# Performance work log

Measured on AMD Instinct MI355X. Metric: run time of the kernel, lower is better.

The kernel has to match this reference:

```python
import jax, jax.numpy as jnp
import numpy as np

B, T, IN_DIM, HID_DIM = 64, 1024, 256, 256


def setup_inputs() -> dict:
    key = jax.random.key(0)
    ks = jax.random.split(key, 5)
    glorot = np.sqrt(6.0 / (IN_DIM + HID_DIM * 2)).astype(np.float32)
    def W(k):
        return jax.random.uniform(k, (IN_DIM + HID_DIM, HID_DIM), jnp.float32, -glorot, glorot)
    return {
        "x": jax.random.normal(ks[0], (B, T, IN_DIM), jnp.float32),
        "W_i": W(ks[1]), "b_i": jnp.zeros((HID_DIM,), jnp.float32),
        "W_f": W(ks[2]), "b_f": jnp.zeros((HID_DIM,), jnp.float32),
        "W_o": W(ks[3]), "b_o": jnp.zeros((HID_DIM,), jnp.float32),
        "W_c": W(ks[4]), "b_c": jnp.zeros((HID_DIM,), jnp.float32),
    }


def reference(x, W_i, b_i, W_f, b_f, W_o, b_o, W_c, b_c):
    # x: [B, T, in_dim] -> time-major [T, B, in_dim]
    xt = jnp.transpose(x, (1, 0, 2))
    batch = x.shape[0]
    c0 = jnp.zeros((batch, HID_DIM), x.dtype)
    h0 = jnp.zeros((batch, HID_DIM), x.dtype)

    def step(carry, x_t):
        c, h = carry
        hx = jnp.concatenate([h, x_t], axis=1)  # [B, hid+in]
        i = jax.nn.sigmoid(hx @ W_i + b_i)
        f = jax.nn.sigmoid(hx @ W_f + b_f)
        o = jax.nn.sigmoid(hx @ W_o + b_o)
        c_new = f * c + i * jnp.tanh(hx @ W_c + b_c)
        h_new = o * jnp.tanh(c_new)
        return (c_new, h_new), h_new

    _, outputs = jax.lax.scan(step, (c0, h0), xt)
    return outputs  # [T, B, hid_dim]
```

## Files before the change

### kernel.cpp

```cpp
#include <hip/hip_runtime.h>
#include <hip/hip_fp16.h>
#include <cstdint>

typedef _Float16 f16x8 __attribute__((ext_vector_type(8)));
typedef _Float16 half2_t __attribute__((ext_vector_type(2)));
typedef float f32x4 __attribute__((ext_vector_type(4)));
typedef uint32_t u32x4 __attribute__((ext_vector_type(4)));
typedef uint32_t u32x2 __attribute__((ext_vector_type(2)));


#define XG_OFF    0ULL
#define XG_BYTES  134217728ULL
#define AP_OFF    (XG_OFF + XG_BYTES)
#define AP_BYTES  33554432ULL
#define BP_OFF    (AP_OFF + AP_BYTES)
#define BP_BYTES  524288ULL
#define WHPQ_OFF  (BP_OFF + BP_BYTES)
#define WHPQ_BYTES 425984ULL
#define WLG_OFF   (WHPQ_OFF + WHPQ_BYTES)
#define WLG_BYTES 98304ULL
#define BIAS_OFF  (WLG_OFF + WLG_BYTES)

__device__ inline half2_t u2h2(uint32_t v) {
    union { uint32_t u; half2_t h; } c; c.u = v; return c.h;
}
#define FD(W, H, A) __builtin_amdgcn_fdot2(u2h2(W), u2h2(H), (A), false)
#define QB(v, pat) __int_as_float(__builtin_amdgcn_ds_swizzle(__float_as_int(v), (pat)))

#define QLIST(F) F(0) F(1) F(2) F(3) F(4) F(5) F(6) F(7) F(8) F(9) F(10) F(11) F(12) \
                 F(13) F(14) F(15) F(16) F(17) F(18) F(19) F(20) F(21) F(22) F(23) F(24) F(25)

__global__ void pack_weights(const float* __restrict__ Wi, const float* __restrict__ Wf,
                             const float* __restrict__ Wo, const float* __restrict__ Wc,
                             const float* __restrict__ bi, const float* __restrict__ bf,
                             const float* __restrict__ bo, const float* __restrict__ bc,
                             uint32_t* __restrict__ WhpQ, uint32_t* __restrict__ WlG,
                             __half* __restrict__ Bp, float* __restrict__ bias_eff)
{
    int tidg = blockIdx.x * blockDim.x + threadIdx.x;
    if (tidg < 106496) {
        int i = tidg & 3;
        int c = (tidg >> 2) & 1023;
        int q = tidg >> 12;
        int kp = q * 4 + i;
        int u = c >> 2, g = c & 3;
        const float* W = (g == 0) ? Wi : (g == 1) ? Wf : (g == 2) ? Wo : Wc;
        union { uint32_t u32; __half h[2]; } pk;
        pk.h[0] = __float2half(W[(2 * kp) * 256 + u]);
        pk.h[1] = __float2half(W[(2 * kp + 1) * 256 + u]);
        WhpQ[tidg] = pk.u32;
    } else if (tidg < 131072) {
        int e = tidg - 106496;
        int k = e & 1;
        int c = (e >> 1) & 1023;
        int jp = e >> 11;
        int kp = 104 + 2 * jp + k;
        int u = c >> 2, g = c & 3;
        const float* W = (g == 0) ? Wi : (g == 1) ? Wf : (g == 2) ? Wo : Wc;
        union { uint32_t u32; __half h[2]; } pk;
        pk.h[0] = __float2half(W[(2 * kp) * 256 + u]);
        pk.h[1] = __float2half(W[(2 * kp + 1) * 256 + u]);
        WlG[e] = pk.u32;
    } else if (tidg < 131072 + 262144) {
        int beta = tidg - 131072;
        int i = beta & 7;
        int l = (beta >> 3) & 63;
        int kk = (beta >> 9) & 7;
        int n = beta >> 12;
        int c = n * 16 + (l & 15);
        int u = c >> 2, g = c & 3;
        int k = kk * 32 + (l >> 4) * 8 + i;
        const float* W = (g == 0) ? Wi : (g == 1) ? Wf : (g == 2) ? Wo : Wc;
        Bp[beta] = __float2half(W[(256 + k) * 256 + u]);
    } else if (tidg < 131072 + 262144 + 1024) {
        int c = tidg - (131072 + 262144);
        int g = c & 3;
        const float* bb = (g == 0) ? bi : (g == 1) ? bf : (g == 2) ? bo : bc;
        bias_eff[c] = bb[c >> 2];
    }
}

__global__ void pack_a(const float* __restrict__ x, __half* __restrict__ Ap)
{
    int t = blockIdx.x * blockDim.x + threadIdx.x;
    int l  = t & 63;
    int kk = (t >> 6) & 7;
    int m  = t >> 9;
    int row = m * 16 + (l & 15);
    int k0  = kk * 32 + (l >> 4) * 8;
    const float* src = x + (size_t)row * 256 + k0;
    f16x8 v;
#pragma unroll
    for (int i = 0; i < 8; ++i) v[i] = (_Float16)src[i];
    *reinterpret_cast<f16x8*>(Ap + (size_t)t * 8) = v;
}

__global__ __launch_bounds__(256) void gemm_xg(const __half* __restrict__ Ap,
                                               const __half* __restrict__ Bp,
                                               const float* __restrict__ bias_eff,
                                               __half* __restrict__ xgh)
{
    int wave = threadIdx.x >> 6;
    int lane = threadIdx.x & 63;
    int mtile = blockIdx.x * 4 + wave;
    int ntbase = blockIdx.y * 16;

    f16x8 a[8];
#pragma unroll
    for (int kk = 0; kk < 8; ++kk)
        a[kk] = *reinterpret_cast<const f16x8*>(Ap + ((size_t)(mtile * 8 + kk) * 64 + lane) * 8);

    int col_lo = lane & 15;
    int rgrp = lane >> 4;
#pragma unroll 1
    for (int j = 0; j < 16; ++j) {
        int nt = ntbase + j;
        int c = nt * 16 + col_lo;
        float bb = bias_eff[c];
        f32x4 acc = {bb, bb, bb, bb};
#pragma unroll
        for (int kk = 0; kk < 8; ++kk) {
            f16x8 bfr = *reinterpret_cast<const f16x8*>(Bp + ((size_t)(nt * 8 + kk) * 64 + lane) * 8);
            acc = __builtin_amdgcn_mfma_f32_16x16x32_f16(a[kk], bfr, acc, 0, 0, 0);
        }
        int hidx = ((c & 511) << 1) | (c >> 9);
#pragma unroll
        for (int r = 0; r < 4; ++r) {
            int row = mtile * 16 + rgrp * 4 + r;
            xgh[(size_t)row * 1024 + hidx] = __float2half(acc[r]);
        }
    }
}

__global__ __launch_bounds__(512, 2) void lstm_rec(
    const uint32_t* __restrict__ xgp,
    const uint32_t* __restrict__ WhpQ,
    const uint32_t* __restrict__ WlG,
    float* __restrict__ out)
{
    const int b = blockIdx.x;
    const int tid = threadIdx.x;
    const int g = tid & 3;
    const int ul = tid >> 2;

    __shared__ uint32_t WlLDS[24576];
    __shared__ alignas(16) uint32_t h2[2][128];

    for (int i = tid; i < 24576; i += 512) WlLDS[i] = WlG[i];
    if (tid < 128) { h2[0][tid] = 0u; h2[1][tid] = 0u; }

#define DECLW(q) u32x4 w0_##q, w1_##q;
    QLIST(DECLW)
#undef DECLW
#define LOADW(q) \
    w0_##q = *reinterpret_cast<const u32x4*>(WhpQ + (((q) * 1024) + tid) * 4); \
    w1_##q = *reinterpret_cast<const u32x4*>(WhpQ + (((q) * 1024) + 512 + tid) * 4);
    QLIST(LOADW)
#undef LOADW
    __syncthreads();

    const float kAct = (g == 3) ? 2.88539008f : -1.44269504f;
    const float aAct = (g == 3) ? -2.0f : 1.0f;
    const float bAct = (g == 3) ? 1.0f : 0.0f;

    float c0s = 0.f, c1s = 0.f;
    const uint32_t* xrow = xgp + (size_t)b * 1024 * 512 + tid;
    uint32_t xw = xrow[0];

    for (int t = 0; t < 1024; ++t) {
        const uint32_t* hr = h2[t & 1];
        int tn = (t < 1023) ? (t + 1) : 1023;
        uint32_t xw_next = xrow[(size_t)tn * 512];

        float a00 = 0.f, a01 = 0.f, a10 = 0.f, a11 = 0.f;
#define DOTQ(q) { \
        u32x4 hq = *reinterpret_cast<const u32x4*>(hr + (q) * 4); \
        a00 = FD(w0_##q[0], hq[0], a00); a10 = FD(w1_##q[0], hq[0], a10); \
        a01 = FD(w0_##q[1], hq[1], a01); a11 = FD(w1_##q[1], hq[1], a11); \
        a00 = FD(w0_##q[2], hq[2], a00); a10 = FD(w1_##q[2], hq[2], a10); \
        a01 = FD(w0_##q[3], hq[3], a01); a11 = FD(w1_##q[3], hq[3], a11); }
        QLIST(DOTQ)
#undef DOTQ

        {
            u32x4 hT0 = *reinterpret_cast<const u32x4*>(hr + 104);
            u32x4 hT1 = *reinterpret_cast<const u32x4*>(hr + 108);
            u32x4 hT2 = *reinterpret_cast<const u32x4*>(hr + 112);
            u32x4 hT3 = *reinterpret_cast<const u32x4*>(hr + 116);
            u32x4 hT4 = *reinterpret_cast<const u32x4*>(hr + 120);
            u32x4 hT5 = *reinterpret_cast<const u32x4*>(hr + 124);
#define TAILJP(jp, HA, HB) { \
            u32x2 wl0 = *reinterpret_cast<const u32x2*>(&WlLDS[((jp) * 1024 + tid) * 2]); \
            u32x2 wl1 = *reinterpret_cast<const u32x2*>(&WlLDS[((jp) * 1024 + 512 + tid) * 2]); \
            a00 = FD(wl0[0], HA, a00); a01 = FD(wl0[1], HB, a01); \
            a10 = FD(wl1[0], HA, a10); a11 = FD(wl1[1], HB, a11); }
            TAILJP(0,  hT0[0], hT0[1])  TAILJP(1,  hT0[2], hT0[3])
            TAILJP(2,  hT1[0], hT1[1])  TAILJP(3,  hT1[2], hT1[3])
            TAILJP(4,  hT2[0], hT2[1])  TAILJP(5,  hT2[2], hT2[3])
            TAILJP(6,  hT3[0], hT3[1])  TAILJP(7,  hT3[2], hT3[3])
            TAILJP(8,  hT4[0], hT4[1])  TAILJP(9,  hT4[2], hT4[3])
            TAILJP(10, hT5[0], hT5[1])  TAILJP(11, hT5[2], hT5[3])
#undef TAILJP
        }

        union { uint32_t u; __half h[2]; } xc; xc.u = xw;
        float pre0 = (a00 + a01) + __half2float(xc.h[0]);
        float pre1 = (a10 + a11) + __half2float(xc.h[1]);

        float r0 = __builtin_amdgcn_rcpf(1.f + __builtin_amdgcn_exp2f(kAct * pre0));
        float r1 = __builtin_amdgcn_rcpf(1.f + __builtin_amdgcn_exp2f(kAct * pre1));
        float gv0 = fmaf(aAct, r0, bAct);
        float gv1 = fmaf(aAct, r1, bAct);

        float i0 = QB(gv0, 0x8000), f0 = QB(gv0, 0x8055), o0 = QB(gv0, 0x80AA), q0 = QB(gv0, 0x80FF);
        float i1 = QB(gv1, 0x8000), f1 = QB(gv1, 0x8055), o1 = QB(gv1, 0x80AA), q1 = QB(gv1, 0x80FF);

        c0s = fmaf(f0, c0s, i0 * q0);
        c1s = fmaf(f1, c1s, i1 * q1);
        float t0 = fmaf(-2.f, __builtin_amdgcn_rcpf(1.f + __builtin_amdgcn_exp2f(2.88539008f * c0s)), 1.f);
        float t1 = fmaf(-2.f, __builtin_amdgcn_rcpf(1.f + __builtin_amdgcn_exp2f(2.88539008f * c1s)), 1.f);
        float h0 = o0 * t0;
        float h1 = o1 * t1;

        __half* hw = reinterpret_cast<__half*>(h2[(t + 1) & 1]);
        if (g == 0)      hw[ul] = __float2half(h0);
        else if (g == 2) hw[128 + ul] = __float2half(h1);
        else if (g == 1) {
            float* orow = out + ((size_t)t * 64 + b) * 256;
            orow[ul] = h0;
            orow[128 + ul] = h1;
        }
        __syncthreads();
        xw = xw_next;
    }
}

extern "C" void kernel_launch(void* const* d_in, const int* in_sizes, int n_in,
                              void* d_out, int out_size, void* d_ws, size_t ws_size,
                              hipStream_t stream)
{
    const float* x  = (const float*)d_in[0];
    const float* Wi = (const float*)d_in[1];
    const float* bi = (const float*)d_in[2];
    const float* Wf = (const float*)d_in[3];
    const float* bf = (const float*)d_in[4];
    const float* Wo = (const float*)d_in[5];
    const float* bo = (const float*)d_in[6];
    const float* Wc = (const float*)d_in[7];
    const float* bc = (const float*)d_in[8];

    char* ws = (char*)d_ws;
    __half*   xgh      = (__half*)(ws + XG_OFF);
    uint32_t* xgp      = (uint32_t*)(ws + XG_OFF);
    __half*   Ap       = (__half*)(ws + AP_OFF);
    __half*   Bp       = (__half*)(ws + BP_OFF);
    uint32_t* WhpQ     = (uint32_t*)(ws + WHPQ_OFF);
    uint32_t* WlG      = (uint32_t*)(ws + WLG_OFF);
    float*    bias_eff = (float*)(ws + BIAS_OFF);

    pack_weights<<<1540, 256, 0, stream>>>(Wi, Wf, Wo, Wc, bi, bf, bo, bc, WhpQ, WlG, Bp, bias_eff);
    pack_a<<<8192, 256, 0, stream>>>(x, Ap);
    gemm_xg<<<dim3(1024, 4), 256, 0, stream>>>(Ap, Bp, bias_eff, xgh);
    lstm_rec<<<64, 512, 0, stream>>>(xgp, WhpQ, WlG, (float*)d_out);
}
```

Measured before the change: 2.362 ms.

## Remap LSTM recurrence to one thread per hidden unit computing all four gates

The recurrent kernel now runs 256 threads per batch row, each owning one hidden unit and all four gate dot products, instead of 512 threads where each handled half the K range for one gate and exchanged gate values via swizzles. Each thread keeps 112 of the 128 packed h-pairs' weights in registers (448 VGPRs, one wave per EU) and reads the remaining 16 from LDS with an XOR-swizzled layout to avoid bank conflicts. This removes the cross-lane gate exchange and halves the number of waves synchronising per step, at the cost of a longer serial dot-product chain per thread and very high register pressure that may spill. The xg layout from the input GEMM is changed to match.

Result: slower. 3.018 ms (+27.8%).

```diff
diff --git a/kernel.cpp b/kernel.cpp
--- a/kernel.cpp
+++ b/kernel.cpp
@@ -15,52 +15,57 @@
 #define AP_BYTES  33554432ULL
 #define BP_OFF    (AP_OFF + AP_BYTES)
 #define BP_BYTES  524288ULL
-#define WHPQ_OFF  (BP_OFF + BP_BYTES)
-#define WHPQ_BYTES 425984ULL
-#define WLG_OFF   (WHPQ_OFF + WHPQ_BYTES)
-#define WLG_BYTES 98304ULL
-#define BIAS_OFF  (WLG_OFF + WLG_BYTES)
+#define WQ_OFF    (BP_OFF + BP_BYTES)
+#define WQ_BYTES  458752ULL
+#define WT_OFF    (WQ_OFF + WQ_BYTES)
+#define WT_BYTES  65536ULL
+#define BIAS_OFF  (WT_OFF + WT_BYTES)
 
 __device__ inline half2_t u2h2(uint32_t v) {
     union { uint32_t u; half2_t h; } c; c.u = v; return c.h;
 }
 #define FD(W, H, A) __builtin_amdgcn_fdot2(u2h2(W), u2h2(H), (A), false)
-#define QB(v, pat) __int_as_float(__builtin_amdgcn_ds_swizzle(__float_as_int(v), (pat)))
-
-#define QLIST(F) F(0) F(1) F(2) F(3) F(4) F(5) F(6) F(7) F(8) F(9) F(10) F(11) F(12) \
-                 F(13) F(14) F(15) F(16) F(17) F(18) F(19) F(20) F(21) F(22) F(23) F(24) F(25)
+
+#define GI4(F, q) F(q,0) F(q,1) F(q,2) F(q,3)
+#define QALL(F) GI4(F,0) GI4(F,1) GI4(F,2) GI4(F,3) GI4(F,4) GI4(F,5) GI4(F,6) \
+  GI4(F,7) GI4(F,8) GI4(F,9) GI4(F,10) GI4(F,11) GI4(F,12) GI4(F,13) GI4(F,14) \
+  GI4(F,15) GI4(F,16) GI4(F,17) GI4(F,18) GI4(F,19) GI4(F,20) GI4(F,21) GI4(F,22) \
+  GI4(F,23) GI4(F,24) GI4(F,25) GI4(F,26) GI4(F,27)
+#define QALL_Q(F) F(0) F(1) F(2) F(3) F(4) F(5) F(6) F(7) F(8) F(9) F(10) F(11) F(12) \
+  F(13) F(14) F(15) F(16) F(17) F(18) F(19) F(20) F(21) F(22) F(23) F(24) F(25) F(26) F(27)
 
 __global__ void pack_weights(const float* __restrict__ Wi, const float* __restrict__ Wf,
                              const float* __restrict__ Wo, const float* __restrict__ Wc,
                              const float* __restrict__ bi, const float* __restrict__ bf,
                              const float* __restrict__ bo, const float* __restrict__ bc,
-                             uint32_t* __restrict__ WhpQ, uint32_t* __restrict__ WlG,
+                             uint32_t* __restrict__ WQg, uint32_t* __restrict__ WTg,
                              __half* __restrict__ Bp, float* __restrict__ bias_eff)
 {
     int tidg = blockIdx.x * blockDim.x + threadIdx.x;
-    if (tidg < 106496) {
-        int i = tidg & 3;
-        int c = (tidg >> 2) & 1023;
-        int q = tidg >> 12;
+    if (tidg < 114688) {
+        int i  = tidg & 3;
+        int gi = (tidg >> 2) & 3;
+        int u  = (tidg >> 4) & 255;
+        int q  = tidg >> 12;
         int kp = q * 4 + i;
-        int u = c >> 2, g = c & 3;
-        const float* W = (g == 0) ? Wi : (g == 1) ? Wf : (g == 2) ? Wo : Wc;
+        const float* W = (gi == 0) ? Wi : (gi == 1) ? Wf : (gi == 2) ? Wo : Wc;
         union { uint32_t u32; __half h[2]; } pk;
         pk.h[0] = __float2half(W[(2 * kp) * 256 + u]);
         pk.h[1] = __float2half(W[(2 * kp + 1) * 256 + u]);
-        WhpQ[tidg] = pk.u32;
+        WQg[tidg] = pk.u32;
     } else if (tidg < 131072) {
-        int e = tidg - 106496;
-        int k = e & 1;
-        int c = (e >> 1) & 1023;
-        int jp = e >> 11;
-        int kp = 104 + 2 * jp + k;
-        int u = c >> 2, g = c & 3;
-        const float* W = (g == 0) ? Wi : (g == 1) ? Wf : (g == 2) ? Wo : Wc;
+        int e  = tidg - 114688;
+        int i  = e & 3;
+        int sl = (e >> 2) & 3;
+        int u  = (e >> 4) & 255;
+        int qt = e >> 12;
+        int gi = sl ^ (u & 3);
+        int kp = 112 + qt * 4 + i;
+        const float* W = (gi == 0) ? Wi : (gi == 1) ? Wf : (gi == 2) ? Wo : Wc;
         union { uint32_t u32; __half h[2]; } pk;
         pk.h[0] = __float2half(W[(2 * kp) * 256 + u]);
         pk.h[1] = __float2half(W[(2 * kp + 1) * 256 + u]);
-        WlG[e] = pk.u32;
+        WTg[e] = pk.u32;
     } else if (tidg < 131072 + 262144) {
         int beta = tidg - 131072;
         int i = beta & 7;
@@ -123,113 +128,99 @@
             f16x8 bfr = *reinterpret_cast<const f16x8*>(Bp + ((size_t)(nt * 8 + kk) * 64 + lane) * 8);
             acc = __builtin_amdgcn_mfma_f32_16x16x32_f16(a[kk], bfr, acc, 0, 0, 0);
         }
-        int hidx = ((c & 511) << 1) | (c >> 9);
 #pragma unroll
         for (int r = 0; r < 4; ++r) {
             int row = mtile * 16 + rgrp * 4 + r;
-            xgh[(size_t)row * 1024 + hidx] = __float2half(acc[r]);
+            xgh[(size_t)row * 1024 + c] = __float2half(acc[r]);
         }
     }
 }
 
-__global__ __launch_bounds__(512, 2) void lstm_rec(
-    const uint32_t* __restrict__ xgp,
-    const uint32_t* __restrict__ WhpQ,
-    const uint32_t* __restrict__ WlG,
-    float* __restrict__ out)
+__global__ __attribute__((amdgpu_flat_work_group_size(256, 256), amdgpu_waves_per_eu(1, 1)))
+void lstm_rec(const __half* __restrict__ xg,
+              const uint32_t* __restrict__ WQg,
+              const uint32_t* __restrict__ WTg,
+              float* __restrict__ out)
 {
     const int b = blockIdx.x;
-    const int tid = threadIdx.x;
-    const int g = tid & 3;
-    const int ul = tid >> 2;
-
-    __shared__ uint32_t WlLDS[24576];
+    const int u = threadIdx.x;
+
+    __shared__ uint32_t WT[16384];
     __shared__ alignas(16) uint32_t h2[2][128];
 
-    for (int i = tid; i < 24576; i += 512) WlLDS[i] = WlG[i];
-    if (tid < 128) { h2[0][tid] = 0u; h2[1][tid] = 0u; }
-
-#define DECLW(q) u32x4 w0_##q, w1_##q;
-    QLIST(DECLW)
+    for (int i = u; i < 4096; i += 256)
+        reinterpret_cast<u32x4*>(WT)[i] = reinterpret_cast<const u32x4*>(WTg)[i];
+    if (u < 128) { h2[0][u] = 0u; h2[1][u] = 0u; }
+
+#define DECLW(q, gi) u32x4 w_##q##_##gi;
+    QALL(DECLW)
 #undef DECLW
-#define LOADW(q) \
-    w0_##q = *reinterpret_cast<const u32x4*>(WhpQ + (((q) * 1024) + tid) * 4); \
-    w1_##q = *reinterpret_cast<const u32x4*>(WhpQ + (((q) * 1024) + 512 + tid) * 4);
-    QLIST(LOADW)
+#define LOADW(q, gi) \
+    w_##q##_##gi = *reinterpret_cast<const u32x4*>(WQg + ((((q) * 256) + u) * 4 + (gi)) * 4);
+    QALL(LOADW)
 #undef LOADW
     __syncthreads();
 
-    const float kAct = (g == 3) ? 2.88539008f : -1.44269504f;
-    const float aAct = (g == 3) ? -2.0f : 1.0f;
-    const float bAct = (g == 3) ? 1.0f : 0.0f;
-
-    float c0s = 0.f, c1s = 0.f;
-    const uint32_t* xrow = xgp + (size_t)b * 1024 * 512 + tid;
-    uint32_t xw = xrow[0];
+    const int m3 = u & 3;
+    const int s0 = (0 ^ m3) * 4, s1 = (1 ^ m3) * 4, s2 = (2 ^ m3) * 4, s3 = (3 ^ m3) * 4;
+
+    float cst = 0.f;
+    const __half* xrow = xg + (size_t)b * 1024 * 1024 + 4 * u;
+    u32x2 xw = *reinterpret_cast<const u32x2*>(xrow);
 
     for (int t = 0; t < 1024; ++t) {
         const uint32_t* hr = h2[t & 1];
         int tn = (t < 1023) ? (t + 1) : 1023;
-        uint32_t xw_next = xrow[(size_t)tn * 512];
-
-        float a00 = 0.f, a01 = 0.f, a10 = 0.f, a11 = 0.f;
+        u32x2 xw_next = *reinterpret_cast<const u32x2*>(xrow + (size_t)tn * 1024);
+
+        float a0 = 0.f, a1 = 0.f, a2 = 0.f, a3 = 0.f;
+#define DOTW(q, gi) \
+        a##gi = FD(w_##q##_##gi[0], hq[0], a##gi); \
+        a##gi = FD(w_##q##_##gi[1], hq[1], a##gi); \
+        a##gi = FD(w_##q##_##gi[2], hq[2], a##gi); \
+        a##gi = FD(w_##q##_##gi[3], hq[3], a##gi);
 #define DOTQ(q) { \
         u32x4 hq = *reinterpret_cast<const u32x4*>(hr + (q) * 4); \
-        a00 = FD(w0_##q[0], hq[0], a00); a10 = FD(w1_##q[0], hq[0], a10); \
-        a01 = FD(w0_##q[1], hq[1], a01); a11 = FD(w1_##q[1], hq[1], a11); \
-        a00 = FD(w0_##q[2], hq[2], a00); a10 = FD(w1_##q[2], hq[2], a10); \
-        a01 = FD(w0_##q[3], hq[3], a01); a11 = FD(w1_##q[3], hq[3], a11); }
-        QLIST(DOTQ)
+        DOTW(q, 0) DOTW(q, 1) DOTW(q, 2) DOTW(q, 3) }
+        QALL_Q(DOTQ)
 #undef DOTQ
-
-        {
-            u32x4 hT0 = *reinterpret_cast<const u32x4*>(hr + 104);
-            u32x4 hT1 = *reinterpret_cast<const u32x4*>(hr + 108);
-            u32x4 hT2 = *reinterpret_cast<const u32x4*>(hr + 112);
-            u32x4 hT3 = *reinterpret_cast<const u32x4*>(hr + 116);
-            u32x4 hT4 = *reinterpret_cast<const u32x4*>(hr + 120);
-            u32x4 hT5 = *reinterpret_cast<const u32x4*>(hr + 124);
-#define TAILJP(jp, HA, HB) { \
-            u32x2 wl0 = *reinterpret_cast<const u32x2*>(&WlLDS[((jp) * 1024 + tid) * 2]); \
-            u32x2 wl1 = *reinterpret_cast<const u32x2*>(&WlLDS[((jp) * 1024 + 512 + tid) * 2]); \
-            a00 = FD(wl0[0], HA, a00); a01 = FD(wl0[1], HB, a01); \
-            a10 = FD(wl1[0], HA, a10); a11 = FD(wl1[1], HB, a11); }
-            TAILJP(0,  hT0[0], hT0[1])  TAILJP(1,  hT0[2], hT0[3])
-            TAILJP(2,  hT1[0], hT1[1])  TAILJP(3,  hT1[2], hT1[3])
-            TAILJP(4,  hT2[0], hT2[1])  TAILJP(5,  hT2[2], hT2[3])
-            TAILJP(6,  hT3[0], hT3[1])  TAILJP(7,  hT3[2], hT3[3])
-            TAILJP(8,  hT4[0], hT4[1])  TAILJP(9,  hT4[2], hT4[3])
-            TAILJP(10, hT5[0], hT5[1])  TAILJP(11, hT5[2], hT5[3])
-#undef TAILJP
-        }
-
-        union { uint32_t u; __half h[2]; } xc; xc.u = xw;
-        float pre0 = (a00 + a01) + __half2float(xc.h[0]);
-        float pre1 = (a10 + a11) + __half2float(xc.h[1]);
-
-        float r0 = __builtin_amdgcn_rcpf(1.f + __builtin_amdgcn_exp2f(kAct * pre0));
-        float r1 = __builtin_amdgcn_rcpf(1.f + __builtin_amdgcn_exp2f(kAct * pre1));
-        float gv0 = fmaf(aAct, r0, bAct);
-        float gv1 = fmaf(aAct, r1, bAct);
-
-        float i0 = QB(gv0, 0x8000), f0 = QB(gv0, 0x8055), o0 = QB(gv0, 0x80AA), q0 = QB(gv0, 0x80FF);
-        float i1 = QB(gv1, 0x8000), f1 = QB(gv1, 0x8055), o1 = QB(gv1, 0x80AA), q1 = QB(gv1, 0x80FF);
-
-        c0s = fmaf(f0, c0s, i0 * q0);
-        c1s = fmaf(f1, c1s, i1 * q1);
-        float t0 = fmaf(-2.f, __builtin_amdgcn_rcpf(1.f + __builtin_amdgcn_exp2f(2.88539008f * c0s)), 1.f);
-        float t1 = fmaf(-2.f, __builtin_amdgcn_rcpf(1.f + __builtin_amdgcn_exp2f(2.88539008f * c1s)), 1.f);
-        float h0 = o0 * t0;
-        float h1 = o1 * t1;
-
-        __half* hw = reinterpret_cast<__half*>(h2[(t + 1) & 1]);
-        if (g == 0)      hw[ul] = __float2half(h0);
-        else if (g == 2) hw[128 + ul] = __float2half(h1);
-        else if (g == 1) {
-            float* orow = out + ((size_t)t * 64 + b) * 256;
-            orow[ul] = h0;
-            orow[128 + ul] = h1;
-        }
+#undef DOTW
+
+#define TAILQ(qt) { \
+        u32x4 hq = *reinterpret_cast<const u32x4*>(hr + 112 + (qt) * 4); \
+        const uint32_t* tb = &WT[(((qt) * 256 + u) * 4) * 4]; \
+        u32x4 wt0 = *reinterpret_cast<const u32x4*>(tb + s0); \
+        u32x4 wt1 = *reinterpret_cast<const u32x4*>(tb + s1); \
+        u32x4 wt2 = *reinterpret_cast<const u32x4*>(tb + s2); \
+        u32x4 wt3 = *reinterpret_cast<const u32x4*>(tb + s3); \
+        a0 = FD(wt0[0], hq[0], a0); a0 = FD(wt0[1], hq[1], a0); \
+        a0 = FD(wt0[2], hq[2], a0); a0 = FD(wt0[3], hq[3], a0); \
+        a1 = FD(wt1[0], hq[0], a1); a1 = FD(wt1[1], hq[1], a1); \
+        a1 = FD(wt1[2], hq[2], a1); a1 = FD(wt1[3], hq[3], a1); \
+        a2 = FD(wt2[0], hq[0], a2); a2 = FD(wt2[1], hq[1], a2); \
+        a2 = FD(wt2[2], hq[2], a2); a2 = FD(wt2[3], hq[3], a2); \
+        a3 = FD(wt3[0], hq[0], a3); a3 = FD(wt3[1], hq[1], a3); \
+        a3 = FD(wt3[2], hq[2], a3); a3 = FD(wt3[3], hq[3], a3); }
+        TAILQ(0) TAILQ(1) TAILQ(2) TAILQ(3)
+#undef TAILQ
+
+        union { u32x2 v; __half h[4]; } xc; xc.v = xw;
+        float pre0 = a0 + __half2float(xc.h[0]);
+        float pre1 = a1 + __half2float(xc.h[1]);
+        float pre2 = a2 + __half2float(xc.h[2]);
+        float pre3 = a3 + __half2float(xc.h[3]);
+
+        float ig = __builtin_amdgcn_rcpf(1.f + __builtin_amdgcn_exp2f(-1.44269504f * pre0));
+        float fg = __builtin_amdgcn_rcpf(1.f + __builtin_amdgcn_exp2f(-1.44269504f * pre1));
+        float og = __builtin_amdgcn_rcpf(1.f + __builtin_amdgcn_exp2f(-1.44269504f * pre2));
+        float cg = fmaf(-2.f, __builtin_amdgcn_rcpf(1.f + __builtin_amdgcn_exp2f(2.88539008f * pre3)), 1.f);
+
+        cst = fmaf(fg, cst, ig * cg);
+        float th = fmaf(-2.f, __builtin_amdgcn_rcpf(1.f + __builtin_amdgcn_exp2f(2.88539008f * cst)), 1.f);
+        float hv = og * th;
+
+        out[((size_t)t * 64 + b) * 256 + u] = hv;
+        reinterpret_cast<__half*>(h2[(t + 1) & 1])[u] = __float2half(hv);
         __syncthreads();
         xw = xw_next;
     }
@@ -251,15 +242,14 @@
 
     char* ws = (char*)d_ws;
     __half*   xgh      = (__half*)(ws + XG_OFF);
-    uint32_t* xgp      = (uint32_t*)(ws + XG_OFF);
     __half*   Ap       = (__half*)(ws + AP_OFF);
     __half*   Bp       = (__half*)(ws + BP_OFF);
-    uint32_t* WhpQ     = (uint32_t*)(ws + WHPQ_OFF);
-    uint32_t* WlG      = (uint32_t*)(ws + WLG_OFF);
+    uint32_t* WQg      = (uint32_t*)(ws + WQ_OFF);
+    uint32_t* WTg      = (uint32_t*)(ws + WT_OFF);
     float*    bias_eff = (float*)(ws + BIAS_OFF);
 
-    pack_weights<<<1540, 256, 0, stream>>>(Wi, Wf, Wo, Wc, bi, bf, bo, bc, WhpQ, WlG, Bp, bias_eff);
+    pack_weights<<<1540, 256, 0, stream>>>(Wi, Wf, Wo, Wc, bi, bf, bo, bc, WQg, WTg, Bp, bias_eff);
     pack_a<<<8192, 256, 0, stream>>>(x, Ap);
     gemm_xg<<<dim3(1024, 4), 256, 0, stream>>>(Ap, Bp, bias_eff, xgh);
-    lstm_rec<<<64, 512, 0, stream>>>(xgp, WhpQ, WlG, (float*)d_out);
-}
+    lstm_rec<<<64, 256, 0, stream>>>(xgh, WQg, WTg, (float*)d_out);
+}
```
